# Kernel optimization log

Hardware: AMD Instinct MI355X
Metric: run time of the kernel (lower is better)

## Reference

```python
import jax, jax.numpy as jnp
import numpy as np

B, S, HID, NH = 2, 2048, 1024, 16
HD = HID // NH  # head_dim = 64


def setup_inputs() -> dict:
    key = jax.random.key(0)
    ks = jax.random.split(key, 11)
    sc = 1.0 / np.sqrt(HID)
    inp = {
        "query": jax.random.normal(ks[0], (B, S, HID), jnp.float32),
        "key_": jax.random.normal(ks[1], (B, S, HID), jnp.float32),
        "value": jax.random.normal(ks[2], (B, S, HID), jnp.float32),
        "Wq": jax.random.normal(ks[3], (HID, HID), jnp.float32) * sc,
        "bq": jnp.zeros((HID,), jnp.float32),
        "Wk": jax.random.normal(ks[4], (HID, HID), jnp.float32) * sc,
        "bk": jnp.zeros((HID,), jnp.float32),
        "Wv": jax.random.normal(ks[5], (HID, HID), jnp.float32) * sc,
        "bv": jnp.zeros((HID,), jnp.float32),
        "Wo": jax.random.normal(ks[6], (HID, HID), jnp.float32) * sc,
        "bo": jnp.zeros((HID,), jnp.float32),
    }
    return inp


def _split_heads(x):
    # [B, S, HID] -> [B, NH, S, HD]
    return x.reshape(B, S, NH, HD).transpose(0, 2, 1, 3)


def reference(query, key_, value, Wq, bq, Wk, bk, Wv, bv, Wo, bo):
    q = _split_heads(query @ Wq + bq)
    k = _split_heads(key_ @ Wk + bk)
    v = _split_heads(value @ Wv + bv)
    scale = 1.0 / jnp.sqrt(jnp.asarray(HD, q.dtype))
    # [B, NH, S, S] scores (unfused attention, as in the original module)
    scores = jnp.einsum("bhqd,bhkd->bhqk", q, k) * scale
    attn = jax.nn.softmax(scores, axis=-1)
    ctx = jnp.einsum("bhqk,bhkd->bhqd", attn, v)  # [B, NH, S, HD]
    ctx = ctx.transpose(0, 2, 1, 3).reshape(B, S, HID)
    return ctx @ Wo + bo
```

## Files before the change

kernel.cpp:

```cpp
#include <hip/hip_runtime.h>


typedef unsigned short u16;
typedef unsigned int u32;
typedef __bf16 bf16x8 __attribute__((ext_vector_type(8)));
typedef float f32x4 __attribute__((ext_vector_type(4)));
typedef u16 u16x4 __attribute__((ext_vector_type(4)));

__device__ __forceinline__ u16 f2bf(float f) {
  __bf16 h = (__bf16)f;
  return *(u16*)&h;
}

__device__ __forceinline__ void gll16(const void* g, void* l) {
  __builtin_amdgcn_global_load_lds(
      (const __attribute__((address_space(1))) u32*)g,
      (__attribute__((address_space(3))) u32*)l, 16, 0, 0);
}

__global__ __launch_bounds__(256) void prep_kernel(
    const float* __restrict__ q32, const float* __restrict__ k32,
    const float* __restrict__ v32,
    u16* __restrict__ qb, u16* __restrict__ kb, u16* __restrict__ vb,
    const float* __restrict__ W0, const float* __restrict__ W1,
    const float* __restrict__ W2, const float* __restrict__ W3,
    u16* __restrict__ T0, u16* __restrict__ T1,
    u16* __restrict__ T2, u16* __restrict__ T3) {
  int blk = blockIdx.x, tid = threadIdx.x;
  if (blk < 12288) {
    int which = blk >> 12;
    const float* in = (which == 0) ? q32 : (which == 1) ? k32 : v32;
    u16* out = (which == 0) ? qb : (which == 1) ? kb : vb;
    int i = (blk & 4095) * 256 + tid;
    float4 v = ((const float4*)in)[i];
    u16x4 o;
    o.x = f2bf(v.x); o.y = f2bf(v.y); o.z = f2bf(v.z); o.w = f2bf(v.w);
    ((u16x4*)out)[i] = o;
  } else {
    int tb = blk - 12288;
    int z = tb >> 10, rest = tb & 1023;
    const float* W = (z == 0) ? W0 : (z == 1) ? W1 : (z == 2) ? W2 : W3;
    u16* WT = (z == 0) ? T0 : (z == 1) ? T1 : (z == 2) ? T2 : T3;
    __shared__ float t[32][33];
    int bx = (rest & 31) * 32, by = (rest >> 5) * 32;
    int tx = tid & 31, ty = tid >> 5;
#pragma unroll
    for (int i = ty; i < 32; i += 8) t[i][tx] = W[(by + i) * 1024 + bx + tx];
    __syncthreads();
#pragma unroll
    for (int i = ty; i < 32; i += 8) WT[(bx + i) * 1024 + by + tx] = f2bf(t[tx][i]);
  }
}

struct GemmJob {
  const u16* A; const u16* BT; const float* bias;
  float* Cf; u16* Cb; int mode; float oscale;
};

template <int BN>
__global__ __launch_bounds__(256, 4) void gemm_sbuf(GemmJob j0, GemmJob j1, GemmJob j2) {
  constexpr int NT = BN / 32;
  constexpr int NBC = BN / 32;
  const int K = 1024, N = 1024;
  __shared__ __align__(16) u16 As[128 * 64];
  __shared__ __align__(16) u16 Bs[BN * 64];
  int blk = blockIdx.x, tid = threadIdx.x;
  int z, r0, bm, bn;
  if (BN == 128) {
    z = blk >> 8; r0 = blk & 255;
    int xcd = r0 & 7, i5 = r0 >> 3;
    bm = (xcd * 4 + (i5 & 3)) * 128;
    bn = (i5 >> 2) * 128;
  } else {
    z = 0; r0 = blk;
    int xcd = r0 & 7, i6 = r0 >> 3;
    bm = (xcd * 4 + (i6 & 3)) * 128;
    bn = (i6 >> 2) * 64;
  }
  GemmJob j = (z == 0) ? j0 : (z == 1) ? j1 : j2;
  int w = tid >> 6, lane = tid & 63, quad = lane >> 4, l16 = lane & 15;
  int wr = (w >> 1) * 64, wc = (w & 1) * (BN / 2);
  f32x4 acc[4][NT] = {};

  auto stage = [&](int kk) {
#pragma unroll
    for (int i = 0; i < 4; ++i) {
      int c = tid + i * 256;
      int r = c >> 3, jp = c & 7, jg = jp ^ (r & 7);
      gll16(&j.A[(size_t)(bm + r) * K + kk + jg * 8], &As[c * 8]);
    }
#pragma unroll
    for (int i = 0; i < NBC; ++i) {
      int c = tid + i * 256;
      int r = c >> 3, jp = c & 7, jg = jp ^ (r & 7);
      gll16(&j.BT[(size_t)(bn + r) * K + kk + jg * 8], &Bs[c * 8]);
    }
  };

  for (int it = 0; it < 16; ++it) {
    __syncthreads();
    stage(it * 64);
    __syncthreads();
#pragma unroll
    for (int ks = 0; ks < 2; ++ks) {
      bf16x8 af[4], bfr[NT];
#pragma unroll
      for (int mt = 0; mt < 4; ++mt) {
        int row = wr + mt * 16 + l16;
        af[mt] = *(const bf16x8*)&As[row * 64 + (((ks * 4 + quad) ^ (row & 7))) * 8];
      }
#pragma unroll
      for (int nt = 0; nt < NT; ++nt) {
        int row = wc + nt * 16 + l16;
        bfr[nt] = *(const bf16x8*)&Bs[row * 64 + (((ks * 4 + quad) ^ (row & 7))) * 8];
      }
#pragma unroll
      for (int mt = 0; mt < 4; ++mt)
#pragma unroll
        for (int nt = 0; nt < NT; ++nt)
          acc[mt][nt] = __builtin_amdgcn_mfma_f32_16x16x32_bf16(af[mt], bfr[nt], acc[mt][nt], 0, 0, 0);
    }
  }

#pragma unroll
  for (int mt = 0; mt < 4; ++mt)
#pragma unroll
    for (int nt = 0; nt < NT; ++nt)
#pragma unroll
      for (int r = 0; r < 4; ++r) {
        int row = bm + wr + mt * 16 + quad * 4 + r;
        int col = bn + wc + nt * 16 + l16;
        float v = (acc[mt][nt][r] + j.bias[col]) * j.oscale;
        if (j.mode == 0) {
          j.Cf[(size_t)row * N + col] = v;
        } else {
          int b = row >> 11, s = row & 2047, h = col >> 6, d = col & 63;
          u16 bv = f2bf(v);
          if (j.mode == 1)
            j.Cb[(((size_t)(b * 16 + h) * 2048 + s) << 6) + d] = bv;
          else
            j.Cb[((size_t)(b * 16 + h) * 64 + d) * 2048 + s] = bv;
        }
      }
}

__global__ __launch_bounds__(256) void attn_kernel(
    const u16* __restrict__ Q,
    const u16* __restrict__ Kk,
    const u16* __restrict__ VT,
    u16* __restrict__ ctx)
{
  __shared__ __align__(16) u16 Ks[2][128 * 64];
  __shared__ __align__(16) u16 Vs[2][64 * 128];

  int blk = blockIdx.x;
  int qt = (blk >> 3) & 15;
  int bh = (blk & 7) * 4 + (blk >> 7);
  int b = bh >> 4, h = bh & 15;
  const u16* Qb = Q + ((size_t)bh * 2048 + qt * 128) * 64;
  const u16* Kb = Kk + (size_t)bh * 2048 * 64;
  const u16* Vb = VT + (size_t)bh * 64 * 2048;
  int tid = threadIdx.x, w = tid >> 6, lane = tid & 63, quad = lane >> 4, l16 = lane & 15;
  int rowbase = w * 32;

  bf16x8 qf[2][2];
#pragma unroll
  for (int f = 0; f < 2; ++f)
#pragma unroll
    for (int ks = 0; ks < 2; ++ks)
      qf[f][ks] = *(const bf16x8*)&Qb[(rowbase + f * 16 + l16) * 64 + ks * 32 + quad * 8];

  f32x4 Oacc[2][4] = {};
  float lacc0 = 0.f, lacc1 = 0.f;

  auto stage = [&](int t, int sel) {
    int kbase = t * 128;
#pragma unroll
    for (int i = 0; i < 4; ++i) {
      int c = tid + i * 256;
      int r = c >> 3, jp = c & 7, jg = jp ^ (r & 7);
      gll16(&Kb[(size_t)(kbase + r) * 64 + jg * 8], &Ks[sel][c * 8]);
    }
#pragma unroll
    for (int i = 0; i < 4; ++i) {
      int c = tid + i * 256;
      int d = c >> 4, jp = c & 15, jg = jp ^ (d & 15);
      gll16(&Vb[(size_t)d * 2048 + kbase + jg * 8], &Vs[sel][c * 8]);
    }
  };

  stage(0, 0);
  __syncthreads();

  for (int kv = 0; kv < 16; ++kv) {
    int cur = kv & 1;
    if (kv < 15) stage(kv + 1, cur ^ 1);

#pragma unroll
    for (int c = 0; c < 4; ++c) {
      f32x4 Sc[2][2] = {};
      __builtin_amdgcn_s_setprio(1);
#pragma unroll
      for (int nt2 = 0; nt2 < 2; ++nt2) {
        int r = (c * 2 + nt2) * 16 + l16;
#pragma unroll
        for (int ks = 0; ks < 2; ++ks) {
          bf16x8 kfr = *(const bf16x8*)&Ks[cur][r * 64 + ((ks * 4 + quad) ^ (l16 & 7)) * 8];
          Sc[0][nt2] = __builtin_amdgcn_mfma_f32_16x16x32_bf16(kfr, qf[0][ks], Sc[0][nt2], 0, 0, 0);
          Sc[1][nt2] = __builtin_amdgcn_mfma_f32_16x16x32_bf16(kfr, qf[1][ks], Sc[1][nt2], 0, 0, 0);
        }
      }
      __builtin_amdgcn_s_setprio(0);

      bf16x8 pf[2];
#pragma unroll
      for (int f = 0; f < 2; ++f) {
        float p0 = __builtin_amdgcn_exp2f(Sc[f][0][0]);
        float p1 = __builtin_amdgcn_exp2f(Sc[f][0][1]);
        float p2 = __builtin_amdgcn_exp2f(Sc[f][0][2]);
        float p3 = __builtin_amdgcn_exp2f(Sc[f][0][3]);
        float p4 = __builtin_amdgcn_exp2f(Sc[f][1][0]);
        float p5 = __builtin_amdgcn_exp2f(Sc[f][1][1]);
        float p6 = __builtin_amdgcn_exp2f(Sc[f][1][2]);
        float p7 = __builtin_amdgcn_exp2f(Sc[f][1][3]);
        float ls = ((p0 + p1) + (p2 + p3)) + ((p4 + p5) + (p6 + p7));
        if (f == 0) lacc0 += ls; else lacc1 += ls;
        u32 u0, u1, u2, u3;
        asm("v_cvt_pk_bf16_f32 %0, %1, %2" : "=v"(u0) : "v"(p0), "v"(p1));
        asm("v_cvt_pk_bf16_f32 %0, %1, %2" : "=v"(u1) : "v"(p2), "v"(p3));
        asm("v_cvt_pk_bf16_f32 %0, %1, %2" : "=v"(u2) : "v"(p4), "v"(p5));
        asm("v_cvt_pk_bf16_f32 %0, %1, %2" : "=v"(u3) : "v"(p6), "v"(p7));
        asm("v_permlane32_swap_b32 %0, %1" : "+v"(u0), "+v"(u2));
        asm("v_permlane32_swap_b32 %0, %1" : "+v"(u1), "+v"(u3));
        asm("v_permlane16_swap_b32 %0, %1" : "+v"(u0), "+v"(u2));
        asm("v_permlane16_swap_b32 %0, %1" : "+v"(u1), "+v"(u3));
        union { u32 u[4]; bf16x8 v; } cv;
        cv.u[0] = u0; cv.u[1] = u1; cv.u[2] = u2; cv.u[3] = u3;
        pf[f] = cv.v;
      }

      __builtin_amdgcn_s_setprio(1);
#pragma unroll
      for (int dt = 0; dt < 4; ++dt) {
        int d = dt * 16 + l16;
        bf16x8 vf = *(const bf16x8*)&Vs[cur][d * 128 + (((c * 4 + quad) ^ l16)) * 8];
        Oacc[0][dt] = __builtin_amdgcn_mfma_f32_16x16x32_bf16(vf, pf[0], Oacc[0][dt], 0, 0, 0);
        Oacc[1][dt] = __builtin_amdgcn_mfma_f32_16x16x32_bf16(vf, pf[1], Oacc[1][dt], 0, 0, 0);
      }
      __builtin_amdgcn_s_setprio(0);
    }

    __syncthreads();
  }

#pragma unroll
  for (int f = 0; f < 2; ++f) {
    float l = (f == 0) ? lacc0 : lacc1;
    l += __shfl_xor(l, 16, 64);
    l += __shfl_xor(l, 32, 64);
    float linv = 1.0f / l;
    int s = qt * 128 + rowbase + f * 16 + l16;
#pragma unroll
    for (int dt = 0; dt < 4; ++dt) {
      u16x4 o;
#pragma unroll
      for (int r = 0; r < 4; ++r) o[r] = f2bf(Oacc[f][dt][r] * linv);
      *(u16x4*)&ctx[(size_t)(b * 2048 + s) * 1024 + h * 64 + dt * 16 + quad * 4] = o;
    }
  }
}


extern "C" void kernel_launch(void* const* d_in, const int* in_sizes, int n_in,
                              void* d_out, int out_size, void* d_ws, size_t ws_size,
                              hipStream_t stream) {
  const float* query = (const float*)d_in[0];
  const float* key_  = (const float*)d_in[1];
  const float* value = (const float*)d_in[2];
  const float* Wq = (const float*)d_in[3];
  const float* bq = (const float*)d_in[4];
  const float* Wk = (const float*)d_in[5];
  const float* bk = (const float*)d_in[6];
  const float* Wv = (const float*)d_in[7];
  const float* bv = (const float*)d_in[8];
  const float* Wo = (const float*)d_in[9];
  const float* bo = (const float*)d_in[10];
  float* out = (float*)d_out;

  char* ws = (char*)d_ws;
  const size_t MB = 1024 * 1024;
  u16* Aq  = (u16*)(ws + 0 * MB);
  u16* Ak  = (u16*)(ws + 8 * MB);
  u16* Av  = (u16*)(ws + 16 * MB);
  u16* WqT = (u16*)(ws + 24 * MB);
  u16* WkT = (u16*)(ws + 26 * MB);
  u16* WvT = (u16*)(ws + 28 * MB);
  u16* WoT = (u16*)(ws + 30 * MB);
  u16* Qp  = (u16*)(ws + 32 * MB);
  u16* Kp  = (u16*)(ws + 40 * MB);
  u16* VTp = (u16*)(ws + 48 * MB);
  u16* Ctx = (u16*)(ws + 56 * MB);

  prep_kernel<<<16384, 256, 0, stream>>>(query, key_, value, Aq, Ak, Av,
                                         Wq, Wk, Wv, Wo, WqT, WkT, WvT, WoT);

  const float sc = 0.125f * 1.44269504f;
  GemmJob jq{Aq, WqT, bq, nullptr, Qp, 1, sc};
  GemmJob jk{Ak, WkT, bk, nullptr, Kp, 1, 1.0f};
  GemmJob jv{Av, WvT, bv, nullptr, VTp, 2, 1.0f};
  gemm_sbuf<128><<<768, 256, 0, stream>>>(jq, jk, jv);

  attn_kernel<<<512, 256, 0, stream>>>(Qp, Kp, VTp, Ctx);

  GemmJob jo{Ctx, WoT, bo, out, nullptr, 0, 1.0f};
  gemm_sbuf<64><<<512, 256, 0, stream>>>(jo, jo, jo);
}
```

Measured before the change: 230.8 us.

## Split attention KV range across two warp groups per block and merge partials

```diff
diff --git a/kernel.cpp b/kernel.cpp
--- a/kernel.cpp
+++ b/kernel.cpp
@@ -144,14 +144,14 @@
       }
 }
 
-__global__ __launch_bounds__(256) void attn_kernel(
+__global__ __launch_bounds__(512, 4) void attn_kernel(
     const u16* __restrict__ Q,
     const u16* __restrict__ Kk,
     const u16* __restrict__ VT,
     u16* __restrict__ ctx)
 {
-  __shared__ __align__(16) u16 Ks[2][128 * 64];
-  __shared__ __align__(16) u16 Vs[2][64 * 128];
+  __shared__ __align__(16) u16 Ks[2][2][64 * 64];
+  __shared__ __align__(16) u16 Vs[2][2][64 * 64];
 
   int blk = blockIdx.x;
   int qt = (blk >> 3) & 15;
@@ -161,7 +161,10 @@
   const u16* Kb = Kk + (size_t)bh * 2048 * 64;
   const u16* Vb = VT + (size_t)bh * 64 * 2048;
   int tid = threadIdx.x, w = tid >> 6, lane = tid & 63, quad = lane >> 4, l16 = lane & 15;
-  int rowbase = w * 32;
+  int g = tid >> 8;
+  int wl = w & 3;
+  int tt = tid & 255;
+  int rowbase = wl * 32;
 
   bf16x8 qf[2][2];
 #pragma unroll
@@ -174,18 +177,18 @@
   float lacc0 = 0.f, lacc1 = 0.f;
 
   auto stage = [&](int t, int sel) {
-    int kbase = t * 128;
-#pragma unroll
-    for (int i = 0; i < 4; ++i) {
-      int c = tid + i * 256;
+    int kbase = g * 1024 + t * 64;
+#pragma unroll
+    for (int i = 0; i < 2; ++i) {
+      int c = tt + i * 256;
       int r = c >> 3, jp = c & 7, jg = jp ^ (r & 7);
-      gll16(&Kb[(size_t)(kbase + r) * 64 + jg * 8], &Ks[sel][c * 8]);
-    }
-#pragma unroll
-    for (int i = 0; i < 4; ++i) {
-      int c = tid + i * 256;
-      int d = c >> 4, jp = c & 15, jg = jp ^ (d & 15);
-      gll16(&Vb[(size_t)d * 2048 + kbase + jg * 8], &Vs[sel][c * 8]);
+      gll16(&Kb[(size_t)(kbase + r) * 64 + jg * 8], &Ks[g][sel][c * 8]);
+    }
+#pragma unroll
+    for (int i = 0; i < 2; ++i) {
+      int c = tt + i * 256;
+      int d = c >> 3, jp = c & 7, jg = jp ^ (d & 7);
+      gll16(&Vb[(size_t)d * 2048 + kbase + jg * 8], &Vs[g][sel][c * 8]);
     }
   };
 
@@ -197,7 +200,7 @@
     if (kv < 15) stage(kv + 1, cur ^ 1);
 
 #pragma unroll
-    for (int c = 0; c < 4; ++c) {
+    for (int c = 0; c < 2; ++c) {
       f32x4 Sc[2][2] = {};
       __builtin_amdgcn_s_setprio(1);
 #pragma unroll
@@ -205,7 +208,7 @@
         int r = (c * 2 + nt2) * 16 + l16;
 #pragma unroll
         for (int ks = 0; ks < 2; ++ks) {
-          bf16x8 kfr = *(const bf16x8*)&Ks[cur][r * 64 + ((ks * 4 + quad) ^ (l16 & 7)) * 8];
+          bf16x8 kfr = *(const bf16x8*)&Ks[g][cur][r * 64 + ((ks * 4 + quad) ^ (l16 & 7)) * 8];
           Sc[0][nt2] = __builtin_amdgcn_mfma_f32_16x16x32_bf16(kfr, qf[0][ks], Sc[0][nt2], 0, 0, 0);
           Sc[1][nt2] = __builtin_amdgcn_mfma_f32_16x16x32_bf16(kfr, qf[1][ks], Sc[1][nt2], 0, 0, 0);
         }
@@ -243,7 +246,7 @@
 #pragma unroll
       for (int dt = 0; dt < 4; ++dt) {
         int d = dt * 16 + l16;
-        bf16x8 vf = *(const bf16x8*)&Vs[cur][d * 128 + (((c * 4 + quad) ^ l16)) * 8];
+        bf16x8 vf = *(const bf16x8*)&Vs[g][cur][d * 64 + (((c * 4 + quad) ^ (l16 & 7))) * 8];
         Oacc[0][dt] = __builtin_amdgcn_mfma_f32_16x16x32_bf16(vf, pf[0], Oacc[0][dt], 0, 0, 0);
         Oacc[1][dt] = __builtin_amdgcn_mfma_f32_16x16x32_bf16(vf, pf[1], Oacc[1][dt], 0, 0, 0);
       }
@@ -253,19 +256,44 @@
     __syncthreads();
   }
 
+  float lred[2];
 #pragma unroll
   for (int f = 0; f < 2; ++f) {
     float l = (f == 0) ? lacc0 : lacc1;
     l += __shfl_xor(l, 16, 64);
     l += __shfl_xor(l, 32, 64);
-    float linv = 1.0f / l;
-    int s = qt * 128 + rowbase + f * 16 + l16;
-#pragma unroll
-    for (int dt = 0; dt < 4; ++dt) {
-      u16x4 o;
-#pragma unroll
-      for (int r = 0; r < 4; ++r) o[r] = f2bf(Oacc[f][dt][r] * linv);
-      *(u16x4*)&ctx[(size_t)(b * 2048 + s) * 1024 + h * 64 + dt * 16 + quad * 4] = o;
+    lred[f] = l;
+  }
+
+  float* ox = (float*)&Ks[0][0][0];
+  float* lx = (float*)&Vs[0][0][0];
+  if (g == 1) {
+#pragma unroll
+    for (int f = 0; f < 2; ++f) {
+#pragma unroll
+      for (int dt = 0; dt < 4; ++dt) {
+        int jc = (dt * 4 + quad) ^ l16;
+        *(f32x4*)&ox[(size_t)(rowbase + f * 16 + l16) * 64 + jc * 4] = Oacc[f][dt];
+      }
+      if (quad == 0) lx[rowbase + f * 16 + l16] = lred[f];
+    }
+  }
+  __syncthreads();
+  if (g == 0) {
+#pragma unroll
+    for (int f = 0; f < 2; ++f) {
+      float lt = lred[f] + lx[rowbase + f * 16 + l16];
+      float linv = 1.0f / lt;
+      int s = qt * 128 + rowbase + f * 16 + l16;
+#pragma unroll
+      for (int dt = 0; dt < 4; ++dt) {
+        int jc = (dt * 4 + quad) ^ l16;
+        f32x4 o1 = *(const f32x4*)&ox[(size_t)(rowbase + f * 16 + l16) * 64 + jc * 4];
+        u16x4 o;
+#pragma unroll
+        for (int r = 0; r < 4; ++r) o[r] = f2bf((Oacc[f][dt][r] + o1[r]) * linv);
+        *(u16x4*)&ctx[(size_t)(b * 2048 + s) * 1024 + h * 64 + dt * 16 + quad * 4] = o;
+      }
     }
   }
 }
@@ -310,7 +338,7 @@
   GemmJob jv{Av, WvT, bv, nullptr, VTp, 2, 1.0f};
   gemm_sbuf<128><<<768, 256, 0, stream>>>(jq, jk, jv);
 
-  attn_kernel<<<512, 256, 0, stream>>>(Qp, Kp, VTp, Ctx);
+  attn_kernel<<<512, 512, 0, stream>>>(Qp, Kp, VTp, Ctx);
 
   GemmJob jo{Ctx, WoT, bo, out, nullptr, 0, 1.0f};
   gemm_sbuf<64><<<512, 256, 0, stream>>>(jo, jo, jo);
```

After: 217.8 us. 1.06x faster.
